# Kernel optimization log

Hardware: AMD Instinct MI355X
Metric: run time of the kernel (lower is better)

The kernel has to match this reference:

```python
import jax, jax.numpy as jnp
import numpy as np

D_MODEL, D_STATE, D_CONV, EXPAND = 768, 16, 4, 2
D_INNER = D_MODEL * EXPAND
B, L = 2, 2048


def setup_inputs() -> dict:
    key = jax.random.key(0)
    ks = jax.random.split(key, 8)

    def xavier(k, shape):
        fan_in, fan_out = shape[0], shape[-1]
        lim = (6.0 / (fan_in + fan_out)) ** 0.5
        return jax.random.uniform(k, shape, jnp.float32, -lim, lim)

    x = jax.random.normal(ks[0], (B, L, D_MODEL), jnp.float32)
    W_in = xavier(ks[1], (D_MODEL, 2 * D_INNER))           # in_proj (no bias)
    W_conv = jax.random.normal(ks[2], (D_INNER, 1, D_CONV), jnp.float32) * 0.1  # depthwise conv kernel
    b_conv = jnp.zeros((D_INNER,), jnp.float32)
    W_x = xavier(ks[3], (D_INNER, 2 * D_STATE))            # x_proj (no bias)
    W_dt = jax.random.normal(ks[4], (D_INNER, D_INNER), jnp.float32) * (1.0 / np.sqrt(D_INNER))
    b_dt = jax.random.uniform(ks[5], (D_INNER,), jnp.float32, 0.001, 0.1)
    A_log = jnp.log(jnp.broadcast_to(jnp.arange(1, D_STATE + 1, dtype=jnp.float32)[None, :], (D_INNER, D_STATE)))
    D = jnp.ones((D_INNER,), jnp.float32)
    W_out = xavier(ks[6], (D_INNER, D_MODEL))              # out_proj (no bias)
    return {"x": x, "W_in": W_in, "W_conv": W_conv, "b_conv": b_conv,
            "W_x": W_x, "W_dt": W_dt, "b_dt": b_dt,
            "A_log": A_log, "D": D, "W_out": W_out}


def reference(x, W_in, W_conv, b_conv, W_x, W_dt, b_dt, A_log, D, W_out):
    Bb, Ll, _ = x.shape
    di = W_conv.shape[0]
    ds = A_log.shape[-1]
    dconv = W_conv.shape[-1]

    xz = x @ W_in                                  # [B,L,2*di]
    x_inner, z = xz[..., :di], xz[..., di:]

    # causal depthwise conv: left-pad d_conv-1, VALID conv (== torch pad+truncate)
    xp = jnp.pad(x_inner.transpose(0, 2, 1), ((0, 0), (0, 0), (dconv - 1, 0)))
    xc = jax.lax.conv_general_dilated(
        xp, W_conv, window_strides=(1,), padding='VALID',
        dimension_numbers=('NCH', 'OIH', 'NCH'), feature_group_count=di)
    xc = (xc + b_conv[None, :, None]).transpose(0, 2, 1)  # [B,L,di]
    xc = jax.nn.silu(xc)

    A = -jnp.exp(A_log)                            # [di,ds]
    BC = xc @ W_x                                  # [B,L,2*ds]
    B_mat, C_mat = BC[..., :ds], BC[..., ds:]
    dt = jax.nn.softplus(xc @ W_dt + b_dt)         # [B,L,di]

    dA = jnp.exp(dt[..., None] * A)                # [B,L,di,ds]
    dBx = dt[..., None] * B_mat[:, :, None, :] * xc[..., None]  # dB * u, [B,L,di,ds]

    def step(h, inp):
        dA_t, dBx_t, C_t = inp                     # [B,di,ds],[B,di,ds],[B,ds]
        h = dA_t * h + dBx_t
        y = jnp.einsum('bdn,bn->bd', h, C_t)
        return h, y

    h0 = jnp.zeros((Bb, di, ds), x.dtype)
    _, ys = jax.lax.scan(step, h0, (dA.transpose(1, 0, 2, 3),
                                    dBx.transpose(1, 0, 2, 3),
                                    C_mat.transpose(1, 0, 2)))
    y = ys.transpose(1, 0, 2)                      # [B,L,di]
    y = (y + xc * D) * jax.nn.silu(z)
    return y @ W_out                               # [B,L,d_model]
```

## Files before the change

### kernel.cpp

```cpp
#include <hip/hip_runtime.h>
#include <hip/hip_bf16.h>
#include <hip/hip_fp16.h>
#include <math.h>

#define DI 1536
#define DM 768
#define DS 16
#define BB 2
#define LL 2048
#define ML (BB*LL)
#define NCHUNK 32
#define CLEN (LL/NCHUNK)
#define NDT 1600

using short8  = __attribute__((ext_vector_type(8))) short;
using floatx4 = __attribute__((ext_vector_type(4))) float;

__device__ __forceinline__ float bf2f(__hip_bfloat16 v) { return __bfloat162float(v); }

__device__ __forceinline__ void async_cp16(const void* g, void* l)
{
    __builtin_amdgcn_global_load_lds(
        (const __attribute__((address_space(1))) unsigned int*)g,
        (__attribute__((address_space(3))) unsigned int*)l,
        16, 0, 0);
}

__global__ __launch_bounds__(256) void cvt_f32_bf16(
    const float* __restrict__ s, __hip_bfloat16* __restrict__ d)
{
    int i = (blockIdx.x * 256 + threadIdx.x) * 4;
    float4 v = *reinterpret_cast<const float4*>(s + i);
    __hip_bfloat16 o[4];
    o[0] = __float2bfloat16(v.x); o[1] = __float2bfloat16(v.y);
    o[2] = __float2bfloat16(v.z); o[3] = __float2bfloat16(v.w);
    *reinterpret_cast<uint2*>(d + i) = *reinterpret_cast<const uint2*>(o);
}

__global__ __launch_bounds__(256) void transpose_f32_bf16(
    const float* __restrict__ src, __hip_bfloat16* __restrict__ dst,
    int R, int C)
{
    __shared__ __hip_bfloat16 tile[32][34];
    int c0 = blockIdx.x * 32, r0 = blockIdx.y * 32;
    int lx = threadIdx.x & 31, ly = threadIdx.x >> 5;
#pragma unroll
    for (int i = 0; i < 4; ++i)
        tile[ly + 8*i][lx] = __float2bfloat16(src[(size_t)(r0 + ly + 8*i) * C + c0 + lx]);
    __syncthreads();
#pragma unroll
    for (int i = 0; i < 4; ++i)
        dst[(size_t)(c0 + ly + 8*i) * R + r0 + lx] = tile[lx][ly + 8*i];
}

template <int EPI, int SK>
__global__ __launch_bounds__(256) void gemm_bf16(
    const __hip_bfloat16* __restrict__ A,
    const __hip_bfloat16* __restrict__ BT,
    void* __restrict__ C0, void* __restrict__ C1, void* __restrict__ C2,
    int M, int N, int K)
{
    __shared__ __hip_bfloat16 As[2][128][32];
    __shared__ __hip_bfloat16 Bs[2][128][32];

    int tid  = threadIdx.x;
    int wave = tid >> 6, lane = tid & 63;
    int quad = lane >> 4, lr = lane & 15;
    int wm = (wave >> 1) * 64, wn = (wave & 1) * 64;
    int bm = blockIdx.x * 128, bn = blockIdx.y * 128;

    floatx4 acc[4][4];
#pragma unroll
    for (int i = 0; i < 4; ++i)
#pragma unroll
        for (int j = 0; j < 4; ++j)
            acc[i][j] = (floatx4){0.f, 0.f, 0.f, 0.f};

    int sr = tid >> 2;
    int sc = (tid & 3) * 8;

    int Klen  = K / SK;
    int kbase = (SK > 1) ? (int)blockIdx.z * Klen : 0;

    const __hip_bfloat16* gA0 = A  + (size_t)(bm + sr)      * K + sc;
    const __hip_bfloat16* gA1 = A  + (size_t)(bm + sr + 64) * K + sc;
    const __hip_bfloat16* gB0 = BT + (size_t)(bn + sr)      * K + sc;
    const __hip_bfloat16* gB1 = BT + (size_t)(bn + sr + 64) * K + sc;

    for (int k0 = kbase; k0 < kbase + Klen; k0 += 64) {
        async_cp16(gA0 + k0,      &As[0][sr][sc]);
        async_cp16(gA0 + k0 + 32, &As[1][sr][sc]);
        async_cp16(gA1 + k0,      &As[0][sr + 64][sc]);
        async_cp16(gA1 + k0 + 32, &As[1][sr + 64][sc]);
        async_cp16(gB0 + k0,      &Bs[0][sr][sc]);
        async_cp16(gB0 + k0 + 32, &Bs[1][sr][sc]);
        async_cp16(gB1 + k0,      &Bs[0][sr + 64][sc]);
        async_cp16(gB1 + k0 + 32, &Bs[1][sr + 64][sc]);
        __syncthreads();

#pragma unroll
        for (int p = 0; p < 2; ++p) {
            short8 afrag[4], bfrag[4];
#pragma unroll
            for (int i = 0; i < 4; ++i)
                afrag[i] = *reinterpret_cast<const short8*>(&As[p][wm + i*16 + lr][quad*8]);
#pragma unroll
            for (int j = 0; j < 4; ++j)
                bfrag[j] = *reinterpret_cast<const short8*>(&Bs[p][wn + j*16 + lr][quad*8]);
#pragma unroll
            for (int i = 0; i < 4; ++i)
#pragma unroll
                for (int j = 0; j < 4; ++j)
                    acc[i][j] = __builtin_amdgcn_mfma_f32_16x16x32_bf16(
                        afrag[i], bfrag[j], acc[i][j], 0, 0, 0);
        }
        __syncthreads();
    }

    float* skOut = nullptr;
    if (EPI == 2)
        skOut = (SK == 1) ? (float*)C0
              : (blockIdx.z == 0 ? (float*)C0 : blockIdx.z == 1 ? (float*)C1 : (float*)C2);

#pragma unroll
    for (int i = 0; i < 4; ++i) {
#pragma unroll
        for (int j = 0; j < 4; ++j) {
            int r0 = bm + wm + i*16 + quad*4;
            int c  = bn + wn + j*16 + lr;
#pragma unroll
            for (int rr = 0; rr < 4; ++rr) {
                float v = acc[i][j][rr];
                if (EPI == 0) {
                    ((__hip_bfloat16*)C0)[(size_t)(r0 + rr) * N + c] = __float2bfloat16(v);
                } else {
                    skOut[(size_t)(r0 + rr) * N + c] = v;
                }
            }
        }
    }
}

__global__ __launch_bounds__(256) void gemm_dt(
    const __hip_bfloat16* __restrict__ A,
    const __hip_bfloat16* __restrict__ BT,
    __half* __restrict__ dtb, float* __restrict__ BC,
    const float* __restrict__ bias,
    int M, int K)
{
    __shared__ __hip_bfloat16 As[128][32];
    __shared__ __hip_bfloat16 Bs[64][32];

    int tid  = threadIdx.x;
    int wave = tid >> 6, lane = tid & 63;
    int quad = lane >> 4, lr = lane & 15;
    int wm = (wave >> 1) * 64, wn = (wave & 1) * 32;
    int bm = blockIdx.x * 128, bn = blockIdx.y * 64;

    floatx4 acc[4][2];
#pragma unroll
    for (int i = 0; i < 4; ++i)
#pragma unroll
        for (int j = 0; j < 2; ++j)
            acc[i][j] = (floatx4){0.f, 0.f, 0.f, 0.f};

    int sr = tid >> 2;
    int sc = (tid & 3) * 8;

    const __hip_bfloat16* gA0 = A  + (size_t)(bm + sr)      * K + sc;
    const __hip_bfloat16* gA1 = A  + (size_t)(bm + sr + 64) * K + sc;
    const __hip_bfloat16* gB0 = BT + (size_t)(bn + sr)      * K + sc;
    __hip_bfloat16* lA0 = &As[sr][sc];
    __hip_bfloat16* lA1 = &As[sr + 64][sc];
    __hip_bfloat16* lB0 = &Bs[sr][sc];

    for (int k0 = 0; k0 < K; k0 += 32) {
        async_cp16(gA0 + k0, lA0);
        async_cp16(gA1 + k0, lA1);
        async_cp16(gB0 + k0, lB0);
        __syncthreads();

        short8 afrag[4], bfrag[2];
#pragma unroll
        for (int i = 0; i < 4; ++i)
            afrag[i] = *reinterpret_cast<const short8*>(&As[wm + i*16 + lr][quad*8]);
#pragma unroll
        for (int j = 0; j < 2; ++j)
            bfrag[j] = *reinterpret_cast<const short8*>(&Bs[wn + j*16 + lr][quad*8]);
#pragma unroll
        for (int i = 0; i < 4; ++i)
#pragma unroll
            for (int j = 0; j < 2; ++j)
                acc[i][j] = __builtin_amdgcn_mfma_f32_16x16x32_bf16(
                    afrag[i], bfrag[j], acc[i][j], 0, 0, 0);
        __syncthreads();
    }

#pragma unroll
    for (int i = 0; i < 4; ++i) {
#pragma unroll
        for (int j = 0; j < 2; ++j) {
            int r0 = bm + wm + i*16 + quad*4;
            int c  = bn + wn + j*16 + lr;
#pragma unroll
            for (int rr = 0; rr < 4; ++rr) {
                float v = acc[i][j][rr];
                if (c < DI) {
                    v += bias[c];
                    float sp = (v > 20.f) ? v : log1pf(__expf(v));
                    dtb[(size_t)(r0 + rr) * DI + c] = __float2half(sp);
                } else if (c < DI + 32) {
                    BC[(size_t)(r0 + rr) * 32 + (c - DI)] = v;
                }
            }
        }
    }
}

__global__ __launch_bounds__(256) void add3(
    float* __restrict__ d, const float* __restrict__ p1, const float* __restrict__ p2)
{
    int i = (blockIdx.x * 256 + threadIdx.x) * 4;
    float4 a = *reinterpret_cast<float4*>(d + i);
    float4 b = *reinterpret_cast<const float4*>(p1 + i);
    float4 c = *reinterpret_cast<const float4*>(p2 + i);
    a.x += b.x + c.x; a.y += b.y + c.y; a.z += b.z + c.z; a.w += b.w + c.w;
    *reinterpret_cast<float4*>(d + i) = a;
}

__global__ __launch_bounds__(256) void conv_silu(
    const __hip_bfloat16* __restrict__ xz,
    const float* __restrict__ Wc,
    const float* __restrict__ bc,
    __hip_bfloat16* __restrict__ xc)
{
    int idx = blockIdx.x * 256 + threadIdx.x;
    int d = (idx % (DI/8)) * 8;
    int m = idx / (DI/8);
    int t = m % LL;
    float acc[8];
#pragma unroll
    for (int h = 0; h < 2; ++h) {
        float4 b4 = *reinterpret_cast<const float4*>(bc + d + h*4);
        acc[h*4+0] = b4.x; acc[h*4+1] = b4.y; acc[h*4+2] = b4.z; acc[h*4+3] = b4.w;
    }
    float4 w[8];
#pragma unroll
    for (int l = 0; l < 8; ++l)
        w[l] = *reinterpret_cast<const float4*>(Wc + (size_t)(d + l) * 4);
#pragma unroll
    for (int j = 0; j < 4; ++j) {
        if (t - 3 + j >= 0) {
            uint4 raw = *reinterpret_cast<const uint4*>(xz + (size_t)(m - 3 + j) * (2*DI) + d);
            __hip_bfloat16 xv[8];
            *reinterpret_cast<uint4*>(xv) = raw;
#pragma unroll
            for (int l = 0; l < 8; ++l)
                acc[l] += bf2f(xv[l]) * ((const float*)&w[l])[j];
        }
    }
    __hip_bfloat16 o[8];
#pragma unroll
    for (int l = 0; l < 8; ++l) {
        float s = acc[l] / (1.f + __expf(-acc[l]));
        o[l] = __float2bfloat16(s);
    }
    *reinterpret_cast<uint4*>(xc + (size_t)m * DI + d) = *reinterpret_cast<const uint4*>(o);
}

__global__ __launch_bounds__(256) void scan_phaseA(
    const __half* __restrict__ dt, const __hip_bfloat16* __restrict__ xc,
    const float* __restrict__ BC, const float* __restrict__ A_log,
    __half* __restrict__ aprod, __half* __restrict__ hend)
{
    int idx = blockIdx.x * 256 + threadIdx.x;
    int q = idx & 3, d = idx >> 2;
    int c = blockIdx.y, b = blockIdx.z;
    float A4[4], h[4], ap[4];
#pragma unroll
    for (int j = 0; j < 4; ++j) {
        A4[j] = -__expf(A_log[d*DS + q*4 + j]);
        h[j] = 0.f; ap[j] = 1.f;
    }
    int t0 = c * CLEN;
    for (int t = t0; t < t0 + CLEN; ++t) {
        size_t row = (size_t)b * LL + t;
        float dtv = __half2float(dt[row * DI + d]);
        float xcv = bf2f(xc[row * DI + d]);
        float4 B4 = *reinterpret_cast<const float4*>(BC + row * 32 + q*4);
        float dtx = dtv * xcv;
#pragma unroll
        for (int j = 0; j < 4; ++j) {
            float dA = __expf(dtv * A4[j]);
            h[j]  = dA * h[j] + ((const float*)&B4)[j] * dtx;
            ap[j] *= dA;
        }
    }
    size_t o = (((size_t)b * NCHUNK + c) * DI + d) * DS + q*4;
    __half oa[4], oh[4];
#pragma unroll
    for (int j = 0; j < 4; ++j) { oa[j] = __float2half(ap[j]); oh[j] = __float2half(h[j]); }
    *reinterpret_cast<uint2*>(aprod + o) = *reinterpret_cast<const uint2*>(oa);
    *reinterpret_cast<uint2*>(hend  + o) = *reinterpret_cast<const uint2*>(oh);
}

__global__ __launch_bounds__(256) void scan_phaseB(
    const __half* __restrict__ aprod, __half* __restrict__ hse)
{
    int idx = blockIdx.x * 256 + threadIdx.x;
    int b = idx / (DI*DS);
    int dn = idx % (DI*DS);
    float H = 0.f;
#pragma unroll
    for (int c = 0; c < NCHUNK; ++c) {
        size_t o = ((size_t)b * NCHUNK + c) * (DI*DS) + dn;
        float a  = __half2float(aprod[o]);
        float he = __half2float(hse[o]);
        hse[o] = __float2half(H);
        H = a * H + he;
    }
}

__global__ __launch_bounds__(256) void scan_phaseC(
    const __half* __restrict__ dt, const __hip_bfloat16* __restrict__ xz,
    const float* __restrict__ BC, const float* __restrict__ A_log,
    const float* __restrict__ Dv, const __half* __restrict__ hstart,
    __hip_bfloat16* __restrict__ xc_y )
{
    int idx = blockIdx.x * 256 + threadIdx.x;
    int q = idx & 3, d = idx >> 2;
    int c = blockIdx.y, b = blockIdx.z;
    float A4[4], h[4];
#pragma unroll
    for (int j = 0; j < 4; ++j)
        A4[j] = -__expf(A_log[d*DS + q*4 + j]);
    float Dd = Dv[d];
    size_t o = (((size_t)b * NCHUNK + c) * DI + d) * DS + q*4;
    {
        uint2 tmp = *reinterpret_cast<const uint2*>(hstart + o);
        const __half* hp = reinterpret_cast<const __half*>(&tmp);
#pragma unroll
        for (int j = 0; j < 4; ++j) h[j] = __half2float(hp[j]);
    }
    int t0 = c * CLEN;
    for (int t = t0; t < t0 + CLEN; ++t) {
        size_t row = (size_t)b * LL + t;
        float dtv = __half2float(dt[row * DI + d]);
        float xcv = bf2f(xc_y[row * DI + d]);
        float zv  = bf2f(xz[row * (2*DI) + DI + d]);
        float4 B4 = *reinterpret_cast<const float4*>(BC + row * 32 + q*4);
        float4 C4 = *reinterpret_cast<const float4*>(BC + row * 32 + 16 + q*4);
        float dtx = dtv * xcv;
        float ys = 0.f;
#pragma unroll
        for (int j = 0; j < 4; ++j) {
            float dA = __expf(dtv * A4[j]);
            h[j] = dA * h[j] + ((const float*)&B4)[j] * dtx;
            ys = fmaf(h[j], ((const float*)&C4)[j], ys);
        }
        ys += __shfl_xor(ys, 1);
        ys += __shfl_xor(ys, 2);
        if (q == 0) {
            float sig = 1.f / (1.f + __expf(-zv));
            float out = (ys + xcv * Dd) * (zv * sig);
            xc_y[row * DI + d] = __float2bfloat16(out);
        }
    }
}

extern "C" void kernel_launch(void* const* d_in, const int* in_sizes, int n_in,
                              void* d_out, int out_size, void* d_ws, size_t ws_size,
                              hipStream_t stream)
{
    const float* x      = (const float*)d_in[0];
    const float* W_in   = (const float*)d_in[1];
    const float* W_conv = (const float*)d_in[2];
    const float* b_conv = (const float*)d_in[3];
    const float* W_x    = (const float*)d_in[4];
    const float* W_dt   = (const float*)d_in[5];
    const float* b_dt   = (const float*)d_in[6];
    const float* A_log  = (const float*)d_in[7];
    const float* Dvec   = (const float*)d_in[8];
    const float* W_out  = (const float*)d_in[9];

    uint8_t* ws = (uint8_t*)d_ws;
    __hip_bfloat16* xz     = (__hip_bfloat16*)(ws);
    float*          p1     = (float*)(ws);
    float*          p2     = (float*)(ws + 12582912);
    __hip_bfloat16* winT   = (__hip_bfloat16*)(ws + 25165824);
    __half*         aprod  = (__half*)(ws + 25165824);
    __half*         hse    = (__half*)(ws + 28311552);
    __hip_bfloat16* wcombT = (__hip_bfloat16*)(ws + 31457280);
    __hip_bfloat16* woutT  = (__hip_bfloat16*)(ws + 31457280);
    __hip_bfloat16* xcb    = (__hip_bfloat16*)(ws + 36569088);
    __half*         dtb    = (__half*)(ws + 49152000);
    __hip_bfloat16* xbf    = (__hip_bfloat16*)(ws + 49152000);
    float*          BC     = (float*)(ws + 61734912);

    cvt_f32_bf16<<<(ML*DM)/1024, 256, 0, stream>>>(x, xbf);
    transpose_f32_bf16<<<dim3(2*DI/32, DM/32), 256, 0, stream>>>(W_in, winT, DM, 2*DI);
    transpose_f32_bf16<<<dim3(DI/32,   DI/32), 256, 0, stream>>>(W_dt, wcombT, DI, DI);
    transpose_f32_bf16<<<dim3(1,       DI/32), 256, 0, stream>>>(W_x,  wcombT + (size_t)DI*DI, DI, 32);

    gemm_bf16<0,1><<<dim3(ML/128, (2*DI)/128), 256, 0, stream>>>(
        xbf, winT, xz, nullptr, nullptr, ML, 2*DI, DM);

    conv_silu<<<(ML*DI/8)/256, 256, 0, stream>>>(xz, W_conv, b_conv, xcb);

    gemm_dt<<<dim3(ML/128, NDT/64), 256, 0, stream>>>(
        xcb, wcombT, dtb, BC, b_dt, ML, DI);

    transpose_f32_bf16<<<dim3(DM/32, DI/32), 256, 0, stream>>>(W_out, woutT, DI, DM);

    scan_phaseA<<<dim3(DI*4/256, NCHUNK, BB), 256, 0, stream>>>(dtb, xcb, BC, A_log, aprod, hse);
    scan_phaseB<<<(BB*DI*DS)/256, 256, 0, stream>>>(aprod, hse);
    scan_phaseC<<<dim3(DI*4/256, NCHUNK, BB), 256, 0, stream>>>(dtb, xz, BC, A_log, Dvec, hse, xcb);

    gemm_bf16<2,3><<<dim3(ML/128, DM/128, 3), 256, 0, stream>>>(
        xcb, woutT, d_out, p1, p2, ML, DM, DI);
    add3<<<(ML*DM)/1024, 256, 0, stream>>>((float*)d_out, p1, p2);

    (void)in_sizes; (void)n_in; (void)out_size; (void)ws_size;
}
```

Before: 329.3 us.

## Double-buffer LDS in GEMM kernels with async prefetch and vmcnt waits

Restructures the main bf16 GEMM and the dt/BC GEMM to keep two LDS buffers, issuing global-to-LDS async copies for the next K-slice while MFMAs run on the current one. The full syncthreads pairs are replaced by explicit s_waitcnt vmcnt plus raw s_barrier, so loads overlap compute. The gemm_dt kernel doubles its LDS footprint, and correctness now depends on the hand-set vmcnt counts matching the number of outstanding copies.

```diff
diff --git a/kernel.cpp b/kernel.cpp
--- a/kernel.cpp
+++ b/kernel.cpp
@@ -26,6 +26,9 @@
         16, 0, 0);
 }
 
+#define WAITCNT_VM(n) asm volatile("s_waitcnt vmcnt(" #n ")" ::: "memory")
+#define PIPE_BARRIER() asm volatile("s_barrier" ::: "memory")
+
 __global__ __launch_bounds__(256) void cvt_f32_bf16(
     const float* __restrict__ s, __hip_bfloat16* __restrict__ d)
 {
@@ -81,40 +84,47 @@
 
     int Klen  = K / SK;
     int kbase = (SK > 1) ? (int)blockIdx.z * Klen : 0;
+    int kend  = kbase + Klen;
 
     const __hip_bfloat16* gA0 = A  + (size_t)(bm + sr)      * K + sc;
     const __hip_bfloat16* gA1 = A  + (size_t)(bm + sr + 64) * K + sc;
     const __hip_bfloat16* gB0 = BT + (size_t)(bn + sr)      * K + sc;
     const __hip_bfloat16* gB1 = BT + (size_t)(bn + sr + 64) * K + sc;
 
-    for (int k0 = kbase; k0 < kbase + Klen; k0 += 64) {
-        async_cp16(gA0 + k0,      &As[0][sr][sc]);
-        async_cp16(gA0 + k0 + 32, &As[1][sr][sc]);
-        async_cp16(gA1 + k0,      &As[0][sr + 64][sc]);
-        async_cp16(gA1 + k0 + 32, &As[1][sr + 64][sc]);
-        async_cp16(gB0 + k0,      &Bs[0][sr][sc]);
-        async_cp16(gB0 + k0 + 32, &Bs[1][sr][sc]);
-        async_cp16(gB1 + k0,      &Bs[0][sr + 64][sc]);
-        async_cp16(gB1 + k0 + 32, &Bs[1][sr + 64][sc]);
-        __syncthreads();
-
-#pragma unroll
-        for (int p = 0; p < 2; ++p) {
-            short8 afrag[4], bfrag[4];
-#pragma unroll
-            for (int i = 0; i < 4; ++i)
-                afrag[i] = *reinterpret_cast<const short8*>(&As[p][wm + i*16 + lr][quad*8]);
+    auto stage = [&](int k0, int b) {
+        async_cp16(gA0 + k0, &As[b][sr][sc]);
+        async_cp16(gA1 + k0, &As[b][sr + 64][sc]);
+        async_cp16(gB0 + k0, &Bs[b][sr][sc]);
+        async_cp16(gB1 + k0, &Bs[b][sr + 64][sc]);
+    };
+    auto compute = [&](int b) {
+        short8 afrag[4], bfrag[4];
+#pragma unroll
+        for (int i = 0; i < 4; ++i)
+            afrag[i] = *reinterpret_cast<const short8*>(&As[b][wm + i*16 + lr][quad*8]);
+#pragma unroll
+        for (int j = 0; j < 4; ++j)
+            bfrag[j] = *reinterpret_cast<const short8*>(&Bs[b][wn + j*16 + lr][quad*8]);
+#pragma unroll
+        for (int i = 0; i < 4; ++i)
 #pragma unroll
             for (int j = 0; j < 4; ++j)
-                bfrag[j] = *reinterpret_cast<const short8*>(&Bs[p][wn + j*16 + lr][quad*8]);
-#pragma unroll
-            for (int i = 0; i < 4; ++i)
-#pragma unroll
-                for (int j = 0; j < 4; ++j)
-                    acc[i][j] = __builtin_amdgcn_mfma_f32_16x16x32_bf16(
-                        afrag[i], bfrag[j], acc[i][j], 0, 0, 0);
-        }
-        __syncthreads();
+                acc[i][j] = __builtin_amdgcn_mfma_f32_16x16x32_bf16(
+                    afrag[i], bfrag[j], acc[i][j], 0, 0, 0);
+    };
+
+    stage(kbase, 0);
+    for (int k0 = kbase; k0 < kend; k0 += 64) {
+        stage(k0 + 32, 1);
+        WAITCNT_VM(4);
+        PIPE_BARRIER();
+        compute(0);
+        PIPE_BARRIER();
+        if (k0 + 64 < kend) { stage(k0 + 64, 0); WAITCNT_VM(4); }
+        else                { WAITCNT_VM(0); }
+        PIPE_BARRIER();
+        compute(1);
+        PIPE_BARRIER();
     }
 
     float* skOut = nullptr;
@@ -148,8 +158,8 @@
     const float* __restrict__ bias,
     int M, int K)
 {
-    __shared__ __hip_bfloat16 As[128][32];
-    __shared__ __hip_bfloat16 Bs[64][32];
+    __shared__ __hip_bfloat16 As[2][128][32];
+    __shared__ __hip_bfloat16 Bs[2][64][32];
 
     int tid  = threadIdx.x;
     int wave = tid >> 6, lane = tid & 63;
@@ -170,30 +180,40 @@
     const __hip_bfloat16* gA0 = A  + (size_t)(bm + sr)      * K + sc;
     const __hip_bfloat16* gA1 = A  + (size_t)(bm + sr + 64) * K + sc;
     const __hip_bfloat16* gB0 = BT + (size_t)(bn + sr)      * K + sc;
-    __hip_bfloat16* lA0 = &As[sr][sc];
-    __hip_bfloat16* lA1 = &As[sr + 64][sc];
-    __hip_bfloat16* lB0 = &Bs[sr][sc];
-
-    for (int k0 = 0; k0 < K; k0 += 32) {
-        async_cp16(gA0 + k0, lA0);
-        async_cp16(gA1 + k0, lA1);
-        async_cp16(gB0 + k0, lB0);
-        __syncthreads();
-
+
+    auto stage = [&](int k0, int b) {
+        async_cp16(gA0 + k0, &As[b][sr][sc]);
+        async_cp16(gA1 + k0, &As[b][sr + 64][sc]);
+        async_cp16(gB0 + k0, &Bs[b][sr][sc]);
+    };
+    auto compute = [&](int b) {
         short8 afrag[4], bfrag[2];
 #pragma unroll
         for (int i = 0; i < 4; ++i)
-            afrag[i] = *reinterpret_cast<const short8*>(&As[wm + i*16 + lr][quad*8]);
+            afrag[i] = *reinterpret_cast<const short8*>(&As[b][wm + i*16 + lr][quad*8]);
 #pragma unroll
         for (int j = 0; j < 2; ++j)
-            bfrag[j] = *reinterpret_cast<const short8*>(&Bs[wn + j*16 + lr][quad*8]);
+            bfrag[j] = *reinterpret_cast<const short8*>(&Bs[b][wn + j*16 + lr][quad*8]);
 #pragma unroll
         for (int i = 0; i < 4; ++i)
 #pragma unroll
             for (int j = 0; j < 2; ++j)
                 acc[i][j] = __builtin_amdgcn_mfma_f32_16x16x32_bf16(
                     afrag[i], bfrag[j], acc[i][j], 0, 0, 0);
-        __syncthreads();
+    };
+
+    stage(0, 0);
+    for (int k0 = 0; k0 < K; k0 += 64) {
+        stage(k0 + 32, 1);
+        WAITCNT_VM(3);
+        PIPE_BARRIER();
+        compute(0);
+        PIPE_BARRIER();
+        if (k0 + 64 < K) { stage(k0 + 64, 0); WAITCNT_VM(3); }
+        else             { WAITCNT_VM(0); }
+        PIPE_BARRIER();
+        compute(1);
+        PIPE_BARRIER();
     }
 
 #pragma unroll
```

Result: slower. 337.9 us (+2.6%).
